# Kernel optimization log

Measured on AMD Instinct MI355X. Metric: run time of the kernel, lower is better.

The kernel has to match this reference:

```python
import jax, jax.numpy as jnp
import numpy as np
import math

D_MODEL = 256
SIGMA = 1.0


def _sinusoidal_pe(L, d_model, dtype=jnp.float32):
    # pe[l, 2i] = sin(l * w_i), pe[l, 2i+1] = cos(l * w_i)
    position = jnp.arange(L, dtype=dtype)[:, None]                       # [L,1]
    div_term = jnp.exp(jnp.arange(0, d_model, 2, dtype=dtype) * (-math.log(10000.0) / d_model))
    pe = jnp.zeros((L, d_model), dtype=dtype)
    pe = pe.at[:, 0::2].set(jnp.sin(position * div_term))
    pe = pe.at[:, 1::2].set(jnp.cos(position * div_term))
    return pe  # [L, d_model]


def setup_inputs() -> dict:
    key = jax.random.key(0)
    # scale 0.05 keeps pairwise sq-distances O(1) so S = exp(-d/2) is non-degenerate
    x = jax.random.normal(key, (4, 4096, 256), dtype=jnp.float32) * 0.05
    return {"x": x}


def reference(x):
    B, L, D = x.shape
    pe = _sinusoidal_pe(L, D_MODEL, dtype=x.dtype)[None]                 # [1,L,D]
    # pairwise squared distances via the expansion ||a||^2+||b||^2-2ab (avoids [B,L,L,D])
    sq = jnp.sum(x * x, axis=-1)                                         # [B,L]
    gram = jnp.einsum('bld,bmd->blm', x, x)                              # [B,L,L]
    dist_sq = jnp.maximum(sq[:, :, None] + sq[:, None, :] - 2.0 * gram, 0.0)
    S = jnp.exp(-dist_sq / (2.0 * SIGMA ** 2))                           # [B,L,L]
    sem = jnp.einsum('blm,bmd->bld', S, x) / jnp.sum(S, axis=-1, keepdims=True)
    return x + pe + sem
```

## Files before the change

kernel.cpp:

```cpp
#include <hip/hip_runtime.h>

typedef unsigned char u8;
typedef float f32x4 __attribute__((ext_vector_type(4)));
typedef float f32x16 __attribute__((ext_vector_type(16)));

#define LL 4096
#define PSTR 136
#define SCALE 16.0f
#define GSCALE (1.0f/256.0f)
#define FREQC (-0.03597789207803197f)

__device__ __forceinline__ long LCAST(uint2 v) { return __builtin_bit_cast(long, v); }

typedef __attribute__((address_space(3))) u8 lds_u8;
typedef __attribute__((address_space(1))) u8 glb_u8;
__device__ __forceinline__ void dma16(const u8* g, u8* l) {
  __builtin_amdgcn_global_load_lds((const glb_u8*)g, (lds_u8*)l, 16, 0, 0);
}

__global__ __launch_bounds__(512) void prep2(const float* __restrict__ x, u8* __restrict__ xbf,
                                             u8* __restrict__ xT, float* __restrict__ sq) {
  __shared__ u8 T2[256 * 72];
  const int blk = blockIdx.x;
  const int b = blk >> 6, ch = blk & 63;
  const int j0 = ch << 6;
  const int tid = threadIdx.x;
  const int wv = tid >> 6, ln = tid & 63;
  const long bL = (long)b * LL;
  const float4* x4 = (const float4*)x + (bL + j0) * 64;
  unsigned* xb4 = (unsigned*)xbf + (bL + j0) * 64;

  #pragma unroll
  for (int g = 0; g < 2; ++g) {
    int pkw[4];
    #pragma unroll
    for (int ii = 0; ii < 4; ++ii) {
      const int row = 8 * wv + 4 * g + ii;
      float4 v = x4[row * 64 + ln];
      float s = v.x * v.x + v.y * v.y + v.z * v.z + v.w * v.w;
      #pragma unroll
      for (int o = 32; o; o >>= 1) s += __shfl_xor(s, o);
      if (ln == 0) sq[bL + j0 + row] = s;
      int pk = __builtin_amdgcn_cvt_pk_fp8_f32(v.x * SCALE, v.y * SCALE, 0, false);
      pk = __builtin_amdgcn_cvt_pk_fp8_f32(v.z * SCALE, v.w * SCALE, pk, true);
      const int sdw = (((ln >> 1) ^ ((j0 + row) & 31)) << 1) | (ln & 1);
      xb4[row * 64 + sdw] = (unsigned)pk;
      pkw[ii] = pk;
    }
    const int rb = 8 * wv + 4 * g;
    #pragma unroll
    for (int k = 0; k < 4; ++k) {
      const unsigned sel = (unsigned)(k | ((4 + k) << 8));
      unsigned m01 = __builtin_amdgcn_perm((unsigned)pkw[1], (unsigned)pkw[0], sel);
      unsigned m23 = __builtin_amdgcn_perm((unsigned)pkw[3], (unsigned)pkw[2], sel);
      unsigned tw  = __builtin_amdgcn_perm(m23, m01, 0x05040100u);
      *(unsigned*)(T2 + (4 * ln + k) * 72 + rb) = tw;
    }
  }
  __syncthreads();
  #pragma unroll
  for (int db = 0; db < 2; ++db) {
    const int d = db * 128 + (tid >> 2);
    const int oct2 = tid & 3;
    const int key = d & 15;
    const int hb = ((ch & 1) << 3) ^ (key & 8);
    const int p0 = hb + 2 * oct2;
    const int c0 = (p0 ^ key) & 7;
    const int c1 = ((p0 + 1) ^ key) & 7;
    uint2 lo = *(const uint2*)(T2 + d * 72 + 8 * c0);
    uint2 hi = *(const uint2*)(T2 + d * 72 + 8 * c1);
    uint4 ov; ov.x = lo.x; ov.y = lo.y; ov.z = hi.x; ov.w = hi.y;
    *(uint4*)(xT + (((long)(b << 8) + d) << 12) + ((ch >> 1) << 7) + (hb << 3) + (oct2 << 4)) = ov;
  }
}

__global__ __launch_bounds__(512, 2) void tpe_main(
    const u8* __restrict__ xbf, const u8* __restrict__ xT,
    const float* __restrict__ sqv,
    const float* __restrict__ x, float* __restrict__ out) {
  __shared__ u8 Kt[2][32768];
  __shared__ u8 Ps[2][64 * PSTR];
  __shared__ float lred[8][64];
  __shared__ float linv[64];

  const int tid = threadIdx.x;
  const int w = tid >> 6;
  const int lane = tid & 63;
  const int l15 = lane & 15, l31 = lane & 31;
  const int q4 = lane >> 4;
  const int q2 = lane >> 5;

  const int blk = blockIdx.x;
  const int b = (blk & 7) >> 1;
  const int qt = ((blk >> 3) << 1) | (blk & 1);
  const int q0 = qt << 6;
  const long bL = (long)b * LL;

  uint2 qf[4][8];
  float qa[4];
  #pragma unroll
  for (int t = 0; t < 4; ++t) {
    const int row = q0 + 16 * t + l15;
    const u8* qrow = xbf + ((bL + row) << 8);
    const int key = row & 31;
    #pragma unroll
    for (int s = 0; s < 8; ++s)
      qf[t][s] = *(const uint2*)(qrow + (((q4 + 4 * s) ^ key) << 3));
    qa[t] = -0.5f * sqv[bL + row];
  }

  f32x16 oacc[2];
  #pragma unroll
  for (int rb = 0; rb < 2; ++rb)
    #pragma unroll
    for (int k = 0; k < 16; ++k) oacc[rb][k] = 0.f;
  float rsacc[4] = {0.f, 0.f, 0.f, 0.f};

  const u8* kbat = xbf + (bL << 8);
  const u8* vseg = xT + (((long)(b << 8) + 32 * w + l31) << 12);
  const int vkey = l31 & 15;

  uint2 vfA[8], vfB[8];

  #pragma unroll
  for (int c = 0; c < 4; ++c) {
    int off = c * 8192 + tid * 16;
    dma16(kbat + off, Kt[0] + off);
  }
  __syncthreads();

#define TPE_ITER(IT, KCUR, KNXT, PPREV, PCUR, VFC, VFN)                                     \
  {                                                                                         \
    const int j0 = (IT) << 7;                                                               \
    if ((IT) < 31) {    \
      const u8* ks = kbat + ((long)((IT) + 1) << 15);                                       \
      _Pragma("unroll")                                                                     \
      for (int c = 0; c < 4; ++c) {                                                         \
        int off = c * 8192 + tid * 16;                                                      \
        dma16(ks + off, (KNXT) + off);                                                      \
      }                                                                                     \
    }                                                                                       \
    float4 skv4 = *(const float4*)(sqv + bL + j0 + 16 * w + 4 * q4);                        \
    if ((IT) != 0) {           \
      _Pragma("unroll")                                                                     \
      for (int s = 0; s < 8; ++s) {                                                         \
        long a0 = *(const long*)((PPREV) + l31 * PSTR + 16 * s + 8 * q2);                   \
        long a1 = *(const long*)((PPREV) + (32 + l31) * PSTR + 16 * s + 8 * q2);            \
        long bv = LCAST(VFC[s]);                                                            \
        oacc[0] = __builtin_amdgcn_mfma_f32_32x32x16_fp8_fp8(a0, bv, oacc[0], 0, 0, 0);     \
        oacc[1] = __builtin_amdgcn_mfma_f32_32x32x16_fp8_fp8(a1, bv, oacc[1], 0, 0, 0);     \
      }                                                                                     \
    }                                                                                       \
    _Pragma("unroll")              \
    for (int s = 0; s < 8; ++s)                                                             \
      VFN[s] = *(const uint2*)(vseg + j0 + (((2 * s + q2) ^ vkey) << 3));                   \
    {                        \
      const int krow = 16 * w + l15;                                                        \
      const int kkey = krow & 31;                                                           \
      const u8* kb2 = (KCUR) + krow * 256;                                                  \
      f32x4 sacc[4];                                                                        \
      _Pragma("unroll")                                                                     \
      for (int t = 0; t < 4; ++t) {                                                         \
        sacc[t][0] = 0.f; sacc[t][1] = 0.f; sacc[t][2] = 0.f; sacc[t][3] = 0.f;             \
      }                                                                                     \
      _Pragma("unroll")                                                                     \
      for (int s = 0; s < 8; ++s) {                                                         \
        uint2 kf = *(const uint2*)(kb2 + (((q4 + 4 * s) ^ kkey) << 3));                     \
        long av = LCAST(kf);                                                                \
        _Pragma("unroll")                                                                   \
        for (int t = 0; t < 4; ++t)                                                         \
          sacc[t] = __builtin_amdgcn_mfma_f32_16x16x32_fp8_fp8(av, LCAST(qf[t][s]), sacc[t], 0, 0, 0); \
      }                                                                                     \
      _Pragma("unroll")        \
      for (int t = 0; t < 4; ++t) {                 \
        float p0 = __expf(fminf(fmaf(sacc[t][0], GSCALE, qa[t] + skv4.x), 0.f));            \
        float p1 = __expf(fminf(fmaf(sacc[t][1], GSCALE, qa[t] + skv4.y), 0.f));            \
        float p2 = __expf(fminf(fmaf(sacc[t][2], GSCALE, qa[t] + skv4.z), 0.f));            \
        float p3 = __expf(fminf(fmaf(sacc[t][3], GSCALE, qa[t] + skv4.w), 0.f));            \
        rsacc[t] += (p0 + p1) + (p2 + p3);                                                  \
        int pk = __builtin_amdgcn_cvt_pk_fp8_f32(p0, p1, 0, false);                         \
        pk = __builtin_amdgcn_cvt_pk_fp8_f32(p2, p3, pk, true);                             \
        *(int*)((PCUR) + (16 * t + l15) * PSTR + 16 * w + 4 * q4) = pk;                     \
      }                                                                                     \
    }                                                                                       \
    __syncthreads();         \
  }

  for (int it2 = 0; it2 < 16; ++it2) {
    TPE_ITER(2 * it2,     Kt[0], Kt[1], Ps[1], Ps[0], vfA, vfB)
    TPE_ITER(2 * it2 + 1, Kt[1], Kt[0], Ps[0], Ps[1], vfB, vfA)
  }
#undef TPE_ITER

  #pragma unroll
  for (int s = 0; s < 8; ++s) {
    long a0 = *(const long*)(Ps[1] + l31 * PSTR + 16 * s + 8 * q2);
    long a1 = *(const long*)(Ps[1] + (32 + l31) * PSTR + 16 * s + 8 * q2);
    long bv = LCAST(vfA[s]);
    oacc[0] = __builtin_amdgcn_mfma_f32_32x32x16_fp8_fp8(a0, bv, oacc[0], 0, 0, 0);
    oacc[1] = __builtin_amdgcn_mfma_f32_32x32x16_fp8_fp8(a1, bv, oacc[1], 0, 0, 0);
  }

  #pragma unroll
  for (int t = 0; t < 4; ++t) {
    float r = rsacc[t];
    r += __shfl_xor(r, 16);
    r += __shfl_xor(r, 32);
    if (lane < 16) lred[w][16 * t + l15] = r;
  }
  __syncthreads();
  if (tid < 64) {
    float s = 0.f;
    #pragma unroll
    for (int ww = 0; ww < 8; ++ww) s += lred[ww][tid];
    linv[tid] = 0.0625f / s;
  }
  __syncthreads();
  const int col = 32 * w + l31;
  const float freq = __expf((float)(col & ~1) * FREQC);
  #pragma unroll
  for (int rb = 0; rb < 2; ++rb) {
    #pragma unroll
    for (int reg = 0; reg < 16; ++reg) {
      int row = 32 * rb + 4 * q2 + (reg & 3) + 8 * (reg >> 2);
      int l = q0 + row;
      float ang = (float)l * freq;
      float pv = (col & 1) ? __cosf(ang) : __sinf(ang);
      long off = ((bL + l) << 8) + col;
      out[off] = oacc[rb][reg] * linv[row] + x[off] + pv;
    }
  }
}

extern "C" void kernel_launch(void* const* d_in, const int* in_sizes, int n_in,
                              void* d_out, int out_size, void* d_ws, size_t ws_size,
                              hipStream_t stream) {
  const float* x = (const float*)d_in[0];
  float* out = (float*)d_out;
  char* ws = (char*)d_ws;
  u8* xbf = (u8*)ws;
  u8* xT = (u8*)(ws + 4194304);
  float* sq = (float*)(ws + 8388608);
  prep2<<<256, 512, 0, stream>>>(x, xbf, xT, sq);
  tpe_main<<<256, 512, 0, stream>>>(xbf, xT, sq, x, out);
}
```

Baseline: 137.7 us.

## Fuse prep and main kernels via cooperative launch with grid sync

Merges the FP8 quantization/transpose prep kernel into the main attention kernel. A cooperative grid-wide sync separates the two phases, and the first Kt LDS buffer is reused as transpose scratch. This removes one kernel launch and the gap between launches. The cost is a grid barrier, and the cooperative launch needs all 256 blocks co-resident, which depends on occupancy.

```diff
diff --git a/kernel.cpp b/kernel.cpp
--- a/kernel.cpp
+++ b/kernel.cpp
@@ -1,4 +1,7 @@
 #include <hip/hip_runtime.h>
+#include <hip/hip_cooperative_groups.h>
+
+namespace cg = cooperative_groups;
 
 typedef unsigned char u8;
 typedef float f32x4 __attribute__((ext_vector_type(4)));
@@ -18,72 +21,73 @@
   __builtin_amdgcn_global_load_lds((const glb_u8*)g, (lds_u8*)l, 16, 0, 0);
 }
 
-__global__ __launch_bounds__(512) void prep2(const float* __restrict__ x, u8* __restrict__ xbf,
-                                             u8* __restrict__ xT, float* __restrict__ sq) {
-  __shared__ u8 T2[256 * 72];
-  const int blk = blockIdx.x;
-  const int b = blk >> 6, ch = blk & 63;
-  const int j0 = ch << 6;
-  const int tid = threadIdx.x;
-  const int wv = tid >> 6, ln = tid & 63;
-  const long bL = (long)b * LL;
-  const float4* x4 = (const float4*)x + (bL + j0) * 64;
-  unsigned* xb4 = (unsigned*)xbf + (bL + j0) * 64;
-
-  #pragma unroll
-  for (int g = 0; g < 2; ++g) {
-    int pkw[4];
-    #pragma unroll
-    for (int ii = 0; ii < 4; ++ii) {
-      const int row = 8 * wv + 4 * g + ii;
-      float4 v = x4[row * 64 + ln];
-      float s = v.x * v.x + v.y * v.y + v.z * v.z + v.w * v.w;
-      #pragma unroll
-      for (int o = 32; o; o >>= 1) s += __shfl_xor(s, o);
-      if (ln == 0) sq[bL + j0 + row] = s;
-      int pk = __builtin_amdgcn_cvt_pk_fp8_f32(v.x * SCALE, v.y * SCALE, 0, false);
-      pk = __builtin_amdgcn_cvt_pk_fp8_f32(v.z * SCALE, v.w * SCALE, pk, true);
-      const int sdw = (((ln >> 1) ^ ((j0 + row) & 31)) << 1) | (ln & 1);
-      xb4[row * 64 + sdw] = (unsigned)pk;
-      pkw[ii] = pk;
-    }
-    const int rb = 8 * wv + 4 * g;
-    #pragma unroll
-    for (int k = 0; k < 4; ++k) {
-      const unsigned sel = (unsigned)(k | ((4 + k) << 8));
-      unsigned m01 = __builtin_amdgcn_perm((unsigned)pkw[1], (unsigned)pkw[0], sel);
-      unsigned m23 = __builtin_amdgcn_perm((unsigned)pkw[3], (unsigned)pkw[2], sel);
-      unsigned tw  = __builtin_amdgcn_perm(m23, m01, 0x05040100u);
-      *(unsigned*)(T2 + (4 * ln + k) * 72 + rb) = tw;
-    }
-  }
-  __syncthreads();
-  #pragma unroll
-  for (int db = 0; db < 2; ++db) {
-    const int d = db * 128 + (tid >> 2);
-    const int oct2 = tid & 3;
-    const int key = d & 15;
-    const int hb = ((ch & 1) << 3) ^ (key & 8);
-    const int p0 = hb + 2 * oct2;
-    const int c0 = (p0 ^ key) & 7;
-    const int c1 = ((p0 + 1) ^ key) & 7;
-    uint2 lo = *(const uint2*)(T2 + d * 72 + 8 * c0);
-    uint2 hi = *(const uint2*)(T2 + d * 72 + 8 * c1);
-    uint4 ov; ov.x = lo.x; ov.y = lo.y; ov.z = hi.x; ov.w = hi.y;
-    *(uint4*)(xT + (((long)(b << 8) + d) << 12) + ((ch >> 1) << 7) + (hb << 3) + (oct2 << 4)) = ov;
-  }
-}
-
-__global__ __launch_bounds__(512, 2) void tpe_main(
-    const u8* __restrict__ xbf, const u8* __restrict__ xT,
-    const float* __restrict__ sqv,
-    const float* __restrict__ x, float* __restrict__ out) {
+__global__ __launch_bounds__(512, 2) void tpe_fused(
+    const float* __restrict__ x, u8* __restrict__ xbf, u8* __restrict__ xT,
+    float* __restrict__ sqv, float* __restrict__ out) {
   __shared__ u8 Kt[2][32768];
   __shared__ u8 Ps[2][64 * PSTR];
   __shared__ float lred[8][64];
   __shared__ float linv[64];
 
   const int tid = threadIdx.x;
+
+  {
+    u8* T2 = Kt[0];
+    const int pblk = blockIdx.x;
+    const int pb = pblk >> 6, ch = pblk & 63;
+    const int j0 = ch << 6;
+    const int wv = tid >> 6, ln = tid & 63;
+    const long pbL = (long)pb * LL;
+    const float4* x4 = (const float4*)x + (pbL + j0) * 64;
+    unsigned* xb4 = (unsigned*)xbf + (pbL + j0) * 64;
+
+    #pragma unroll
+    for (int g = 0; g < 2; ++g) {
+      int pkw[4];
+      #pragma unroll
+      for (int ii = 0; ii < 4; ++ii) {
+        const int row = 8 * wv + 4 * g + ii;
+        float4 v = x4[row * 64 + ln];
+        float s = v.x * v.x + v.y * v.y + v.z * v.z + v.w * v.w;
+        #pragma unroll
+        for (int o = 32; o; o >>= 1) s += __shfl_xor(s, o);
+        if (ln == 0) sqv[pbL + j0 + row] = s;
+        int pk = __builtin_amdgcn_cvt_pk_fp8_f32(v.x * SCALE, v.y * SCALE, 0, false);
+        pk = __builtin_amdgcn_cvt_pk_fp8_f32(v.z * SCALE, v.w * SCALE, pk, true);
+        const int sdw = (((ln >> 1) ^ ((j0 + row) & 31)) << 1) | (ln & 1);
+        xb4[row * 64 + sdw] = (unsigned)pk;
+        pkw[ii] = pk;
+      }
+      const int rb = 8 * wv + 4 * g;
+      #pragma unroll
+      for (int k = 0; k < 4; ++k) {
+        const unsigned sel = (unsigned)(k | ((4 + k) << 8));
+        unsigned m01 = __builtin_amdgcn_perm((unsigned)pkw[1], (unsigned)pkw[0], sel);
+        unsigned m23 = __builtin_amdgcn_perm((unsigned)pkw[3], (unsigned)pkw[2], sel);
+        unsigned tw  = __builtin_amdgcn_perm(m23, m01, 0x05040100u);
+        *(unsigned*)(T2 + (4 * ln + k) * 72 + rb) = tw;
+      }
+    }
+    __syncthreads();
+    #pragma unroll
+    for (int db = 0; db < 2; ++db) {
+      const int d = db * 128 + (tid >> 2);
+      const int oct2 = tid & 3;
+      const int key = d & 15;
+      const int hb = ((ch & 1) << 3) ^ (key & 8);
+      const int p0 = hb + 2 * oct2;
+      const int c0 = (p0 ^ key) & 7;
+      const int c1 = ((p0 + 1) ^ key) & 7;
+      uint2 lo = *(const uint2*)(T2 + d * 72 + 8 * c0);
+      uint2 hi = *(const uint2*)(T2 + d * 72 + 8 * c1);
+      uint4 ov; ov.x = lo.x; ov.y = lo.y; ov.z = hi.x; ov.w = hi.y;
+      *(uint4*)(xT + (((long)(pb << 8) + d) << 12) + ((ch >> 1) << 7) + (hb << 3) + (oct2 << 4)) = ov;
+    }
+  }
+
+  __threadfence();
+  cg::this_grid().sync();
+
   const int w = tid >> 6;
   const int lane = tid & 63;
   const int l15 = lane & 15, l31 = lane & 31;
@@ -241,6 +245,7 @@
   u8* xbf = (u8*)ws;
   u8* xT = (u8*)(ws + 4194304);
   float* sq = (float*)(ws + 8388608);
-  prep2<<<256, 512, 0, stream>>>(x, xbf, xT, sq);
-  tpe_main<<<256, 512, 0, stream>>>(xbf, xT, sq, x, out);
+  void* args[5] = {(void*)&x, (void*)&xbf, (void*)&xT, (void*)&sq, (void*)&out};
+  hipLaunchCooperativeKernel(reinterpret_cast<void*>(tpe_fused), dim3(256), dim3(512),
+                             args, 0, stream);
 }
```

Measured after the change: 233.2 us. 69.4% more time.

## Halve query tile to 32 rows with 256-thread blocks and 512 blocks

Applied to the files above, without the earlier changes.

The attention-like kernel now processes 32 query rows per block with 4 waves instead of 64 rows with 8 waves, and streams 64-key chunks instead of 128. The grid doubles to 512 blocks, so more blocks are available across the CUs and LDS per block shrinks. Each wave now owns 64 output columns, using two V fragments per P fragment. In exchange, K and V tiles are reused across fewer query rows, so total K/V traffic doubles, and the number of barriers and loop iterations doubles.

```diff
diff --git a/kernel.cpp b/kernel.cpp
--- a/kernel.cpp
+++ b/kernel.cpp
@@ -5,7 +5,7 @@
 typedef float f32x16 __attribute__((ext_vector_type(16)));
 
 #define LL 4096
-#define PSTR 136
+#define PSTR 72
 #define SCALE 16.0f
 #define GSCALE (1.0f/256.0f)
 #define FREQC (-0.03597789207803197f)
@@ -74,14 +74,14 @@
   }
 }
 
-__global__ __launch_bounds__(512, 2) void tpe_main(
+__global__ __launch_bounds__(256, 2) void tpe_main(
     const u8* __restrict__ xbf, const u8* __restrict__ xT,
     const float* __restrict__ sqv,
     const float* __restrict__ x, float* __restrict__ out) {
-  __shared__ u8 Kt[2][32768];
-  __shared__ u8 Ps[2][64 * PSTR];
-  __shared__ float lred[8][64];
-  __shared__ float linv[64];
+  __shared__ u8 Kt[2][16384];
+  __shared__ u8 Ps[2][32 * PSTR];
+  __shared__ float lred[4][32];
+  __shared__ float linv[32];
 
   const int tid = threadIdx.x;
   const int w = tid >> 6;
@@ -93,13 +93,13 @@
   const int blk = blockIdx.x;
   const int b = (blk & 7) >> 1;
   const int qt = ((blk >> 3) << 1) | (blk & 1);
-  const int q0 = qt << 6;
+  const int q0 = qt << 5;
   const long bL = (long)b * LL;
 
-  uint2 qf[4][8];
-  float qa[4];
-  #pragma unroll
-  for (int t = 0; t < 4; ++t) {
+  uint2 qf[2][8];
+  float qa[2];
+  #pragma unroll
+  for (int t = 0; t < 2; ++t) {
     const int row = q0 + 16 * t + l15;
     const u8* qrow = xbf + ((bL + row) << 8);
     const int key = row & 31;
@@ -111,56 +111,62 @@
 
   f32x16 oacc[2];
   #pragma unroll
-  for (int rb = 0; rb < 2; ++rb)
-    #pragma unroll
-    for (int k = 0; k < 16; ++k) oacc[rb][k] = 0.f;
-  float rsacc[4] = {0.f, 0.f, 0.f, 0.f};
+  for (int db = 0; db < 2; ++db)
+    #pragma unroll
+    for (int k = 0; k < 16; ++k) oacc[db][k] = 0.f;
+  float rsacc[2] = {0.f, 0.f};
 
   const u8* kbat = xbf + (bL << 8);
-  const u8* vseg = xT + (((long)(b << 8) + 32 * w + l31) << 12);
+  const u8* vseg0 = xT + (((long)(b << 8) + 64 * w + l31) << 12);
+  const u8* vseg1 = vseg0 + (32l << 12);
   const int vkey = l31 & 15;
 
-  uint2 vfA[8], vfB[8];
+  uint2 vfA[2][4], vfB[2][4];
 
   #pragma unroll
   for (int c = 0; c < 4; ++c) {
-    int off = c * 8192 + tid * 16;
+    int off = c * 4096 + tid * 16;
     dma16(kbat + off, Kt[0] + off);
   }
   __syncthreads();
 
 #define TPE_ITER(IT, KCUR, KNXT, PPREV, PCUR, VFC, VFN)                                     \
   {                                                                                         \
-    const int j0 = (IT) << 7;                                                               \
-    if ((IT) < 31) {    \
-      const u8* ks = kbat + ((long)((IT) + 1) << 15);                                       \
+    const int j0 = (IT) << 6;                                                               \
+    if ((IT) < 63) {    \
+      const u8* ks = kbat + ((long)((IT) + 1) << 14);                                       \
       _Pragma("unroll")                                                                     \
       for (int c = 0; c < 4; ++c) {                                                         \
-        int off = c * 8192 + tid * 16;                                                      \
+        int off = c * 4096 + tid * 16;                                                      \
         dma16(ks + off, (KNXT) + off);                                                      \
       }                                                                                     \
     }                                                                                       \
     float4 skv4 = *(const float4*)(sqv + bL + j0 + 16 * w + 4 * q4);                        \
     if ((IT) != 0) {           \
       _Pragma("unroll")                                                                     \
-      for (int s = 0; s < 8; ++s) {                                                         \
+      for (int s = 0; s < 4; ++s) {                                                         \
         long a0 = *(const long*)((PPREV) + l31 * PSTR + 16 * s + 8 * q2);                   \
-        long a1 = *(const long*)((PPREV) + (32 + l31) * PSTR + 16 * s + 8 * q2);            \
-        long bv = LCAST(VFC[s]);                                                            \
-        oacc[0] = __builtin_amdgcn_mfma_f32_32x32x16_fp8_fp8(a0, bv, oacc[0], 0, 0, 0);     \
-        oacc[1] = __builtin_amdgcn_mfma_f32_32x32x16_fp8_fp8(a1, bv, oacc[1], 0, 0, 0);     \
-      }                                                                                     \
-    }                                                                                       \
-    _Pragma("unroll")              \
-    for (int s = 0; s < 8; ++s)                                                             \
-      VFN[s] = *(const uint2*)(vseg + j0 + (((2 * s + q2) ^ vkey) << 3));                   \
+        oacc[0] = __builtin_amdgcn_mfma_f32_32x32x16_fp8_fp8(a0, LCAST(VFC[0][s]), oacc[0], 0, 0, 0); \
+        oacc[1] = __builtin_amdgcn_mfma_f32_32x32x16_fp8_fp8(a0, LCAST(VFC[1][s]), oacc[1], 0, 0, 0); \
+      }                                                                                     \
+    }                                                                                       \
+    {           \
+      const int segoff = ((IT) >> 1) << 7;                                                  \
+      const int chb = ((IT) & 1) << 3;                                                      \
+      _Pragma("unroll")                                                                     \
+      for (int s = 0; s < 4; ++s) {                                                         \
+        const int co = (((chb | (2 * s + q2)) ^ vkey) << 3);                                \
+        VFN[0][s] = *(const uint2*)(vseg0 + segoff + co);                                   \
+        VFN[1][s] = *(const uint2*)(vseg1 + segoff + co);                                   \
+      }                                                                                     \
+    }                                                                                       \
     {                        \
       const int krow = 16 * w + l15;                                                        \
       const int kkey = krow & 31;                                                           \
       const u8* kb2 = (KCUR) + krow * 256;                                                  \
-      f32x4 sacc[4];                                                                        \
-      _Pragma("unroll")                                                                     \
-      for (int t = 0; t < 4; ++t) {                                                         \
+      f32x4 sacc[2];                                                                        \
+      _Pragma("unroll")                                                                     \
+      for (int t = 0; t < 2; ++t) {                                                         \
         sacc[t][0] = 0.f; sacc[t][1] = 0.f; sacc[t][2] = 0.f; sacc[t][3] = 0.f;             \
       }                                                                                     \
       _Pragma("unroll")                                                                     \
@@ -168,11 +174,11 @@
         uint2 kf = *(const uint2*)(kb2 + (((q4 + 4 * s) ^ kkey) << 3));                     \
         long av = LCAST(kf);                                                                \
         _Pragma("unroll")                                                                   \
-        for (int t = 0; t < 4; ++t)                                                         \
+        for (int t = 0; t < 2; ++t)                                                         \
           sacc[t] = __builtin_amdgcn_mfma_f32_16x16x32_fp8_fp8(av, LCAST(qf[t][s]), sacc[t], 0, 0, 0); \
       }                                                                                     \
       _Pragma("unroll")        \
-      for (int t = 0; t < 4; ++t) {                 \
+      for (int t = 0; t < 2; ++t) {                 \
         float p0 = __expf(fminf(fmaf(sacc[t][0], GSCALE, qa[t] + skv4.x), 0.f));            \
         float p1 = __expf(fminf(fmaf(sacc[t][1], GSCALE, qa[t] + skv4.y), 0.f));            \
         float p2 = __expf(fminf(fmaf(sacc[t][2], GSCALE, qa[t] + skv4.z), 0.f));            \
@@ -186,48 +192,46 @@
     __syncthreads();         \
   }
 
-  for (int it2 = 0; it2 < 16; ++it2) {
+  for (int it2 = 0; it2 < 32; ++it2) {
     TPE_ITER(2 * it2,     Kt[0], Kt[1], Ps[1], Ps[0], vfA, vfB)
     TPE_ITER(2 * it2 + 1, Kt[1], Kt[0], Ps[0], Ps[1], vfB, vfA)
   }
 #undef TPE_ITER
 
   #pragma unroll
-  for (int s = 0; s < 8; ++s) {
+  for (int s = 0; s < 4; ++s) {
     long a0 = *(const long*)(Ps[1] + l31 * PSTR + 16 * s + 8 * q2);
-    long a1 = *(const long*)(Ps[1] + (32 + l31) * PSTR + 16 * s + 8 * q2);
-    long bv = LCAST(vfA[s]);
-    oacc[0] = __builtin_amdgcn_mfma_f32_32x32x16_fp8_fp8(a0, bv, oacc[0], 0, 0, 0);
-    oacc[1] = __builtin_amdgcn_mfma_f32_32x32x16_fp8_fp8(a1, bv, oacc[1], 0, 0, 0);
-  }
-
-  #pragma unroll
-  for (int t = 0; t < 4; ++t) {
+    oacc[0] = __builtin_amdgcn_mfma_f32_32x32x16_fp8_fp8(a0, LCAST(vfA[0][s]), oacc[0], 0, 0, 0);
+    oacc[1] = __builtin_amdgcn_mfma_f32_32x32x16_fp8_fp8(a0, LCAST(vfA[1][s]), oacc[1], 0, 0, 0);
+  }
+
+  #pragma unroll
+  for (int t = 0; t < 2; ++t) {
     float r = rsacc[t];
     r += __shfl_xor(r, 16);
     r += __shfl_xor(r, 32);
     if (lane < 16) lred[w][16 * t + l15] = r;
   }
   __syncthreads();
-  if (tid < 64) {
+  if (tid < 32) {
     float s = 0.f;
     #pragma unroll
-    for (int ww = 0; ww < 8; ++ww) s += lred[ww][tid];
+    for (int ww = 0; ww < 4; ++ww) s += lred[ww][tid];
     linv[tid] = 0.0625f / s;
   }
   __syncthreads();
-  const int col = 32 * w + l31;
-  const float freq = __expf((float)(col & ~1) * FREQC);
-  #pragma unroll
-  for (int rb = 0; rb < 2; ++rb) {
+  #pragma unroll
+  for (int db = 0; db < 2; ++db) {
+    const int col = 64 * w + 32 * db + l31;
+    const float freq = __expf((float)(col & ~1) * FREQC);
     #pragma unroll
     for (int reg = 0; reg < 16; ++reg) {
-      int row = 32 * rb + 4 * q2 + (reg & 3) + 8 * (reg >> 2);
+      int row = 4 * q2 + (reg & 3) + 8 * (reg >> 2);
       int l = q0 + row;
       float ang = (float)l * freq;
       float pv = (col & 1) ? __cosf(ang) : __sinf(ang);
       long off = ((bL + l) << 8) + col;
-      out[off] = oacc[rb][reg] * linv[row] + x[off] + pv;
+      out[off] = oacc[db][reg] * linv[row] + x[off] + pv;
     }
   }
 }
@@ -242,5 +246,5 @@
   u8* xT = (u8*)(ws + 4194304);
   float* sq = (float*)(ws + 8388608);
   prep2<<<256, 512, 0, stream>>>(x, xbf, xT, sq);
-  tpe_main<<<256, 512, 0, stream>>>(xbf, xT, sq, x, out);
-}
+  tpe_main<<<512, 256, 0, stream>>>(xbf, xT, sq, x, out);
+}
```

Measured after the change: 182.1 us. 32.3% more time.
